# Performance work log

Measured on AMD Instinct MI355X. Metric: run time of the kernel, lower is better.

## Reference

```python
import jax, jax.numpy as jnp
import numpy as np

NV, NR = 30000, 1000
EVV, EVI, EIV = 400000, 120000, 120000
VD, RD, ED = 16, 8, 2
HID, OUT, H1 = 64, 64, 2


def _seg_softmax(logits, seg, n):
    # numerically stable segment softmax over destination nodes
    m = jax.ops.segment_max(logits, seg, num_segments=n)
    m = jnp.where(jnp.isfinite(m), m, 0.0)
    ex = jnp.exp(logits - m[seg])
    den = jax.ops.segment_sum(ex, seg, num_segments=n)
    return ex / (den[seg] + 1e-16)


def _gatv2(x_src, x_dst, src, dst, ea, Wl, Wr, We, att, b, heads, n_dst, concat):
    # PyG GATv2Conv: e = att . leaky_relu(Wl x_j + Wr x_i + We e_ij); out = sum_j softmax(e) * Wl x_j
    C = att.shape[-1]
    hl = (x_src @ Wl).reshape(-1, heads, C)
    hr = (x_dst @ Wr).reshape(-1, heads, C)
    he = (ea @ We).reshape(-1, heads, C)
    xj = hl[src]                                   # [E, H, C]
    g = jax.nn.leaky_relu(xj + hr[dst] + he, 0.2)
    logits = jnp.einsum('ehc,hc->eh', g, att)      # [E, H]
    alpha = _seg_softmax(logits, dst, n_dst)
    out = jax.ops.segment_sum(xj * alpha[..., None], dst, num_segments=n_dst)
    out = out.reshape(n_dst, heads * C) if concat else out.mean(axis=1)
    return out + b


def _self_loops(src, dst, ea, n):
    # PyG add_self_loops(fill_value='mean'): self-loop edge_attr = per-dst mean of incoming edge_attr
    deg = jax.ops.segment_sum(jnp.ones((ea.shape[0],), ea.dtype), dst, num_segments=n)
    mean = jax.ops.segment_sum(ea, dst, num_segments=n) / jnp.maximum(deg, 1.0)[:, None]
    ar = jnp.arange(n, dtype=src.dtype)
    return jnp.concatenate([src, ar]), jnp.concatenate([dst, ar]), jnp.concatenate([ea, mean], axis=0)


def _ln(x, g, b):
    m = x.mean(-1, keepdims=True)
    v = ((x - m) ** 2).mean(-1, keepdims=True)
    return (x - m) * jax.lax.rsqrt(v + 1e-5) * g + b


def setup_inputs() -> dict:
    key = jax.random.key(0)
    ks = iter(jax.random.split(key, 80))
    def rn(shape, s=1.0):
        return jax.random.normal(next(ks), shape, jnp.float32) * s
    def ri(n, hi):
        return jax.random.randint(next(ks), (n,), 0, hi, jnp.int32)
    d = {'x_veh': rn((NV, VD)), 'x_rsu': rn((NR, RD)),
         'ea_v2v': rn((EVV, ED)), 'ea_v2i': rn((EVI, ED)), 'ea_i2v': rn((EIV, ED)),
         'src_v2v': ri(EVV, NV), 'dst_v2v': ri(EVV, NV),
         'src_v2i': ri(EVI, NV), 'dst_v2i': ri(EVI, NR),
         'src_i2v': ri(EIV, NR), 'dst_i2v': ri(EIV, NV)}
    H1C = H1 * HID
    for rel, di_s, di_d in (('vv', VD, VD), ('vi', VD, RD), ('iv', RD, VD)):
        d['Wl_' + rel + '1'] = rn((di_s, H1C), 0.1)
        d['Wr_' + rel + '1'] = rn((di_d, H1C), 0.1)
        d['We_' + rel + '1'] = rn((ED, H1C), 0.1)
        d['att_' + rel + '1'] = rn((H1, HID), 0.1)
        d['b_' + rel + '1'] = jnp.zeros((H1C,), jnp.float32)
    for rel in ('vv', 'vi', 'iv'):
        d['Wl_' + rel + '2'] = rn((H1C, OUT), 0.1)
        d['Wr_' + rel + '2'] = rn((H1C, OUT), 0.1)
        d['We_' + rel + '2'] = rn((ED, OUT), 0.1)
        d['att_' + rel + '2'] = rn((1, OUT), 0.1)
        d['b_' + rel + '2'] = jnp.zeros((OUT,), jnp.float32)
    d['ln_vg'] = jnp.ones((OUT,), jnp.float32)
    d['ln_vb'] = jnp.zeros((OUT,), jnp.float32)
    d['ln_rg'] = jnp.ones((OUT,), jnp.float32)
    d['ln_rb'] = jnp.zeros((OUT,), jnp.float32)
    return d


def reference(x_veh, x_rsu, ea_v2v, ea_v2i, ea_i2v,
              src_v2v, dst_v2v, src_v2i, dst_v2i, src_i2v, dst_i2v,
              Wl_vv1, Wr_vv1, We_vv1, att_vv1, b_vv1,
              Wl_vi1, Wr_vi1, We_vi1, att_vi1, b_vi1,
              Wl_iv1, Wr_iv1, We_iv1, att_iv1, b_iv1,
              Wl_vv2, Wr_vv2, We_vv2, att_vv2, b_vv2,
              Wl_vi2, Wr_vi2, We_vi2, att_vi2, b_vi2,
              Wl_iv2, Wr_iv2, We_iv2, att_iv2, b_iv2,
              ln_vg, ln_vb, ln_rg, ln_rb):
    s_vv, d_vv, ea_vv = _self_loops(src_v2v, dst_v2v, ea_v2v, NV)
    # layer 1 (heads=2, concat=True), HeteroConv aggr='sum'
    v1 = (_gatv2(x_veh, x_veh, s_vv, d_vv, ea_vv, Wl_vv1, Wr_vv1, We_vv1, att_vv1, b_vv1, H1, NV, True)
          + _gatv2(x_rsu, x_veh, src_i2v, dst_i2v, ea_i2v, Wl_iv1, Wr_iv1, We_iv1, att_iv1, b_iv1, H1, NV, True))
    r1 = _gatv2(x_veh, x_rsu, src_v2i, dst_v2i, ea_v2i, Wl_vi1, Wr_vi1, We_vi1, att_vi1, b_vi1, H1, NR, True)
    v1 = jax.nn.elu(v1)
    r1 = jax.nn.elu(r1)
    # layer 2 (heads=1, concat=False -> mean over 1 head)
    v2 = (_gatv2(v1, v1, s_vv, d_vv, ea_vv, Wl_vv2, Wr_vv2, We_vv2, att_vv2, b_vv2, 1, NV, False)
          + _gatv2(r1, v1, src_i2v, dst_i2v, ea_i2v, Wl_iv2, Wr_iv2, We_iv2, att_iv2, b_iv2, 1, NV, False))
    r2 = _gatv2(v1, r1, src_v2i, dst_v2i, ea_v2i, Wl_vi2, Wr_vi2, We_vi2, att_vi2, b_vi2, 1, NR, False)
    return jnp.concatenate([_ln(v2, ln_vg, ln_vb), _ln(r2, ln_rg, ln_rb)], axis=0)
```

## Files before the change

### kernel.cpp

```cpp
#include <hip/hip_runtime.h>
#include <hip/hip_fp16.h>

constexpr int NV = 30000, NR = 1000;
constexpr int EVV = 400000, EVI = 120000, EIV = 120000;
constexpr int ETOT = EVV + EIV + EVI;
constexpr int VB = (NV + 3) / 4;
constexpr float LOFF = 4.0f;

struct __align__(8) Edge { int s; __half2 ea; };
typedef __half2 h2;

__device__ __forceinline__ h2 h2shfl_xor(h2 v, int m) {
  int i = *(int*)&v;
  i = __shfl_xor(i, m);
  return *(h2*)&i;
}
__device__ __forceinline__ h2 h2max(h2 a, h2 b) {
  h2 r;
  asm("v_pk_max_f16 %0, %1, %2" : "=v"(r) : "v"(a), "v"(b));
  return r;
}

constexpr size_t OFF_CNT_VV = 0;
constexpr size_t OFF_CUR_VV = OFF_CNT_VV + NV;
constexpr size_t OFF_CNT_IV = OFF_CUR_VV + NV;
constexpr size_t OFF_CUR_IV = OFF_CNT_IV + NV;
constexpr size_t OFF_CNT_VI = OFF_CUR_IV + NV;
constexpr size_t OFF_CUR_VI = OFF_CNT_VI + NR;
constexpr size_t ZERO_END   = OFF_CUR_VI + NR;
constexpr size_t OFF_PTR_VV = ZERO_END;
constexpr size_t OFF_PTR_IV = OFF_PTR_VV + NV + 2;
constexpr size_t OFF_PTR_VI = OFF_PTR_IV + NV + 2;
constexpr size_t OFF_E_VV   = OFF_PTR_VI + NR + 2;
constexpr size_t OFF_E_IV   = OFF_E_VV + (size_t)EVV * 2;
constexpr size_t OFF_E_VI   = OFF_E_IV + (size_t)EIV * 2;
constexpr size_t OFF_H      = (OFF_E_VI + (size_t)EVI * 2 + 3) & ~(size_t)3;
constexpr size_t OFF_HL_VV1 = OFF_H;
constexpr size_t OFF_HR_VV1 = OFF_HL_VV1 + (size_t)NV * 64;
constexpr size_t OFF_HR_IV1 = OFF_HR_VV1 + (size_t)NV * 64;
constexpr size_t OFF_HL_VI1 = OFF_HR_IV1 + (size_t)NV * 64;
constexpr size_t OFF_HL_IV1 = OFF_HL_VI1 + (size_t)NV * 64;
constexpr size_t OFF_HR_VI1 = OFF_HL_IV1 + (size_t)NR * 64;
constexpr size_t L1_END     = OFF_HR_VI1 + (size_t)NR * 64;
constexpr size_t OFF_V1     = L1_END;
constexpr size_t OFF_R1     = OFF_V1 + (size_t)NV * 64;
constexpr size_t WS_END     = OFF_R1 + (size_t)NR * 64;
constexpr size_t OFF_HL_VV2 = OFF_H;
constexpr size_t OFF_HR_VV2 = OFF_HL_VV2 + (size_t)NV * 32;
constexpr size_t OFF_HR_IV2 = OFF_HR_VV2 + (size_t)NV * 32;
constexpr size_t OFF_HL_VI2 = OFF_HR_IV2 + (size_t)NV * 32;
constexpr size_t OFF_HL_IV2 = OFF_HL_VI2 + (size_t)NV * 32;
constexpr size_t OFF_HR_VI2 = OFF_HL_IV2 + (size_t)NR * 32;
constexpr size_t L2_END     = OFF_HR_VI2 + (size_t)NR * 32;
static_assert(L2_END <= OFF_V1, "layer-2 overlay must not clobber v1/r1");

__global__ __launch_bounds__(256) void k_count3(
    const int* __restrict__ dvv, const int* __restrict__ div_, const int* __restrict__ dvi,
    int* __restrict__ cvv, int* __restrict__ civ, int* __restrict__ cvi) {
  int t = blockIdx.x * blockDim.x + threadIdx.x;
  if (t < EVV) atomicAdd(&cvv[dvv[t]], 1);
  else if (t < EVV + EIV) atomicAdd(&civ[div_[t - EVV]], 1);
  else if (t < ETOT) atomicAdd(&cvi[dvi[t - EVV - EIV]], 1);
}

__global__ __launch_bounds__(1024) void k_scan3(
    const int* c0, int* p0, int n0,
    const int* c1, int* p1, int n1,
    const int* c2, int* p2, int n2) {
  const int* cnt = blockIdx.x == 0 ? c0 : blockIdx.x == 1 ? c1 : c2;
  int* ptr = blockIdx.x == 0 ? p0 : blockIdx.x == 1 ? p1 : p2;
  int n = blockIdx.x == 0 ? n0 : blockIdx.x == 1 ? n1 : n2;
  __shared__ int tsum[1024];
  int t = threadIdx.x;
  int per = (n + 1023) >> 10;
  int base = t * per;
  int s = 0;
  for (int i = 0; i < per; i++) { int idx = base + i; if (idx < n) s += cnt[idx]; }
  tsum[t] = s;
  for (int off = 1; off < 1024; off <<= 1) {
    __syncthreads();
    int v = (t >= off) ? tsum[t - off] : 0;
    __syncthreads();
    tsum[t] += v;
  }
  __syncthreads();
  int run = tsum[t] - s;
  for (int i = 0; i < per; i++) {
    int idx = base + i;
    if (idx < n) { ptr[idx] = run; run += cnt[idx]; }
  }
  if (t == 1023) ptr[n] = tsum[1023];
}

__global__ __launch_bounds__(256) void k_fill3(
    const int* __restrict__ svv, const int* __restrict__ dvv, const float* __restrict__ eavv,
    const int* __restrict__ siv, const int* __restrict__ div_, const float* __restrict__ eaiv,
    const int* __restrict__ svi, const int* __restrict__ dvi, const float* __restrict__ eavi,
    const int* __restrict__ pvv, int* __restrict__ uvv, Edge* __restrict__ evv,
    const int* __restrict__ piv, int* __restrict__ uiv, Edge* __restrict__ eiv,
    const int* __restrict__ pvi, int* __restrict__ uvi, Edge* __restrict__ evi) {
  int t = blockIdx.x * blockDim.x + threadIdx.x;
  if (t < EVV) {
    int e = t, d = dvv[e];
    int idx = pvv[d] + atomicAdd(&uvv[d], 1);
    Edge ed; ed.s = svv[e]; ed.ea = __floats2half2_rn(eavv[2 * e], eavv[2 * e + 1]);
    evv[idx] = ed;
  } else if (t < EVV + EIV) {
    int e = t - EVV, d = div_[e];
    int idx = piv[d] + atomicAdd(&uiv[d], 1);
    Edge ed; ed.s = siv[e]; ed.ea = __floats2half2_rn(eaiv[2 * e], eaiv[2 * e + 1]);
    eiv[idx] = ed;
  } else if (t < ETOT) {
    int e = t - EVV - EIV, d = dvi[e];
    int idx = pvi[d] + atomicAdd(&uvi[d], 1);
    Edge ed; ed.s = svi[e]; ed.ea = __floats2half2_rn(eavi[2 * e], eavi[2 * e + 1]);
    evi[idx] = ed;
  }
}

template<int K, int NW>
__global__ __launch_bounds__(256) void k_gemm1(const float* __restrict__ X,
    const float* __restrict__ W0, const float* __restrict__ W1,
    const float* __restrict__ W2, const float* __restrict__ W3,
    __half* __restrict__ Y0, __half* __restrict__ Y1,
    __half* __restrict__ Y2, __half* __restrict__ Y3, int n) {
  constexpr int ROWS = 8;
  __shared__ float xs[ROWS][K];
  int r0 = blockIdx.x * ROWS;
  int tid = threadIdx.x;
  int col = tid & 127, grp = tid >> 7;
  for (int i = tid; i < ROWS * K; i += 256) {
    int gi = r0 * K + i;
    ((float*)xs)[i] = (gi < n * K) ? X[gi] : 0.f;
  }
  __syncthreads();
  int oidx = ((col & 63) << 1) + (col >> 6);
#pragma unroll
  for (int rep = 0; rep < NW / 2; rep++) {
    int wi = grp + rep * 2;
    const float* __restrict__ W = wi == 0 ? W0 : wi == 1 ? W1 : wi == 2 ? W2 : W3;
    __half* __restrict__ Y = wi == 0 ? Y0 : wi == 1 ? Y1 : wi == 2 ? Y2 : Y3;
    float acc[ROWS];
#pragma unroll
    for (int r = 0; r < ROWS; r++) acc[r] = 0.f;
#pragma unroll
    for (int k4 = 0; k4 < K / 4; k4++) {
      float w0 = W[(4 * k4 + 0) * 128 + col];
      float w1 = W[(4 * k4 + 1) * 128 + col];
      float w2 = W[(4 * k4 + 2) * 128 + col];
      float w3 = W[(4 * k4 + 3) * 128 + col];
#pragma unroll
      for (int r = 0; r < ROWS; r++) {
        float4 x4 = *(const float4*)&xs[r][4 * k4];
        acc[r] = fmaf(x4.x, w0, acc[r]);
        acc[r] = fmaf(x4.y, w1, acc[r]);
        acc[r] = fmaf(x4.z, w2, acc[r]);
        acc[r] = fmaf(x4.w, w3, acc[r]);
      }
    }
#pragma unroll
    for (int r = 0; r < ROWS; r++)
      if (r0 + r < n) Y[(size_t)(r0 + r) * 128 + oidx] = __float2half(acc[r]);
  }
}

template<int NW>
__global__ __launch_bounds__(64 * NW) void k_gemm2(const __half* __restrict__ X,
    const float* __restrict__ W0, const float* __restrict__ W1,
    const float* __restrict__ W2, const float* __restrict__ W3,
    __half* __restrict__ Y0, __half* __restrict__ Y1,
    __half* __restrict__ Y2, __half* __restrict__ Y3, int n) {
  constexpr int ROWS = 16, K = 128;
  __shared__ float xs[ROWS][K];
  int r0 = blockIdx.x * ROWS;
  int tid = threadIdx.x;
  const __half2* X2 = (const __half2*)X;
  for (int i = tid; i < ROWS * K / 2; i += 64 * NW) {
    int gi = r0 * (K / 2) + i;
    float2 f = (gi < n * (K / 2)) ? __half22float2(X2[gi]) : make_float2(0.f, 0.f);
    ((float*)xs)[2 * i] = f.x;
    ((float*)xs)[2 * i + 1] = f.y;
  }
  __syncthreads();
  int lane = tid & 63, wv = tid >> 6;
  const float* __restrict__ W = wv == 0 ? W0 : wv == 1 ? W1 : wv == 2 ? W2 : W3;
  __half* __restrict__ Y = wv == 0 ? Y0 : wv == 1 ? Y1 : wv == 2 ? Y2 : Y3;
  float acc[ROWS];
#pragma unroll
  for (int r = 0; r < ROWS; r++) acc[r] = 0.f;
  for (int k4 = 0; k4 < K / 4; k4++) {
    float w0 = W[(4 * k4 + 0) * 64 + lane];
    float w1 = W[(4 * k4 + 1) * 64 + lane];
    float w2 = W[(4 * k4 + 2) * 64 + lane];
    float w3 = W[(4 * k4 + 3) * 64 + lane];
#pragma unroll
    for (int r = 0; r < ROWS; r++) {
      float4 x4 = *(const float4*)&xs[r][4 * k4];
      acc[r] = fmaf(x4.x, w0, acc[r]);
      acc[r] = fmaf(x4.y, w1, acc[r]);
      acc[r] = fmaf(x4.z, w2, acc[r]);
      acc[r] = fmaf(x4.w, w3, acc[r]);
    }
  }
#pragma unroll
  for (int r = 0; r < ROWS; r++)
    if (r0 + r < n) Y[(size_t)(r0 + r) * 64 + lane] = __float2half(acc[r]);
}


template<bool SELF>
__device__ __forceinline__ void gatW2(int d, int lane, int eg, int cg,
    int b, int cnt,
    const Edge* __restrict__ ed,
    const __half* __restrict__ hl, const __half* __restrict__ hr,
    const float* __restrict__ We, const float* __restrict__ att,
    float* acc, float& den0, float& den1) {
  h2 hrc2[4], av2[4], w02[4], w12[4];
  {
    float4 r = *(const float4*)&hr[(size_t)d * 128 + cg * 8];
    const h2* hp = (const h2*)&r;
#pragma unroll
    for (int j = 0; j < 4; j++) hrc2[j] = hp[j];
  }
#pragma unroll
  for (int j = 0; j < 4; j++) {
    int c = cg * 4 + j;
    av2[j] = __floats2half2_rn(att[c], att[64 + c]);
    w02[j] = __floats2half2_rn(We[c], We[64 + c]);
    w12[j] = __floats2half2_rn(We[128 + c], We[192 + c]);
  }
  const h2 c02 = __float2half2_rn(0.2f);
  h2 acc2[4];
#pragma unroll
  for (int j = 0; j < 4; j++) acc2[j] = __float2half2_rn(0.f);
  float sum0 = 0.f, sum1 = 0.f;
  auto proc = [&](float4 r, int eab, bool v) {
    const h2* hp = (const h2*)&r;
    h2 eh = *(h2*)&eab;
    h2 ef0 = __low2half2(eh), ef1 = __high2half2(eh);
    h2 lacc = __float2half2_rn(0.f);
#pragma unroll
    for (int j = 0; j < 4; j++) {
      h2 g = __hfma2(ef0, w02[j], __hadd2(hp[j], hrc2[j]));
      g = __hfma2(ef1, w12[j], g);
      h2 lr = h2max(g, __hmul2(c02, g));
      lacc = __hfma2(lr, av2[j], lacc);
    }
#pragma unroll
    for (int o = 1; o <= 8; o <<= 1) lacc = __hadd2(lacc, h2shfl_xor(lacc, o));
    float2 lf = __half22float2(lacc);
    float ex0 = v ? __expf(lf.x - LOFF) : 0.f;
    float ex1 = v ? __expf(lf.y - LOFF) : 0.f;
    h2 exh = __floats2half2_rn(ex0, ex1);
#pragma unroll
    for (int j = 0; j < 4; j++) acc2[j] = __hfma2(exh, hp[j], acc2[j]);
    den0 += ex0; den1 += ex1;
  };
  for (int wf = 0; wf < cnt; wf += 64) {
    int idx = wf + lane;
    int es = 0, eab = 0;
    if (idx < cnt) { Edge e = ed[b + idx]; es = e.s; eab = *(const int*)&e.ea; }
    if (SELF) {
      float2 f = __half22float2(*(h2*)&eab);
      sum0 += f.x; sum1 += f.y;
    }
    int wlen = min(64, cnt - wf);
    int kk = 0;
    for (; kk + 16 <= wlen; kk += 16) {
      int k0 = kk + eg, k1 = kk + 4 + eg, k2 = kk + 8 + eg, k3 = kk + 12 + eg;
      int s0 = __shfl(es, k0), ea0 = __shfl(eab, k0);
      int s1 = __shfl(es, k1), ea1 = __shfl(eab, k1);
      int s2 = __shfl(es, k2), ea2 = __shfl(eab, k2);
      int s3 = __shfl(es, k3), ea3 = __shfl(eab, k3);
      float4 r0 = *(const float4*)&hl[(size_t)s0 * 128 + cg * 8];
      float4 r1 = *(const float4*)&hl[(size_t)s1 * 128 + cg * 8];
      float4 r2 = *(const float4*)&hl[(size_t)s2 * 128 + cg * 8];
      float4 r3 = *(const float4*)&hl[(size_t)s3 * 128 + cg * 8];
      proc(r0, ea0, true);
      proc(r1, ea1, true);
      proc(r2, ea2, true);
      proc(r3, ea3, true);
    }
    for (; kk < wlen; kk += 4) {
      int k0 = kk + eg;
      int s0 = __shfl(es, k0), ea0 = __shfl(eab, k0);
      float4 r0 = *(const float4*)&hl[(size_t)s0 * 128 + cg * 8];
      proc(r0, ea0, k0 < wlen);
    }
  }
  if (SELF) {
#pragma unroll
    for (int o = 1; o <= 32; o <<= 1) { sum0 += __shfl_xor(sum0, o); sum1 += __shfl_xor(sum1, o); }
    float dg = fmaxf((float)cnt, 1.f);
    __half2 mh = __floats2half2_rn(sum0 / dg, sum1 / dg);
    int meab = *(const int*)&mh;
    float4 rS = *(const float4*)&hl[(size_t)d * 128 + cg * 8];
    proc(rS, meab, eg == 0);
  }
#pragma unroll
  for (int o = 16; o <= 32; o <<= 1) {
#pragma unroll
    for (int j = 0; j < 4; j++) acc2[j] = __hadd2(acc2[j], h2shfl_xor(acc2[j], o));
    den0 += __shfl_xor(den0, o);
    den1 += __shfl_xor(den1, o);
  }
#pragma unroll
  for (int j = 0; j < 4; j++) {
    float2 f = __half22float2(acc2[j]);
    acc[2 * j] = f.x; acc[2 * j + 1] = f.y;
  }
}

template<bool SELF>
__device__ __forceinline__ void gatW1(int d, int lane, int eg8, int cg8,
    int b, int cnt,
    const Edge* __restrict__ ed,
    const __half* __restrict__ hl, const __half* __restrict__ hr,
    const float* __restrict__ We, const float* __restrict__ att,
    float* acc, float& den) {
  h2 hrc2[4], av2[4], w02[4], w12[4];
  {
    float4 r = *(const float4*)&hr[(size_t)d * 64 + cg8 * 8];
    const h2* hp = (const h2*)&r;
#pragma unroll
    for (int j = 0; j < 4; j++) hrc2[j] = hp[j];
  }
#pragma unroll
  for (int j = 0; j < 4; j++) {
    int c = cg8 * 8 + 2 * j;
    av2[j] = __floats2half2_rn(att[c], att[c + 1]);
    w02[j] = __floats2half2_rn(We[c], We[c + 1]);
    w12[j] = __floats2half2_rn(We[64 + c], We[64 + c + 1]);
  }
  const h2 c02 = __float2half2_rn(0.2f);
  h2 acc2[4];
#pragma unroll
  for (int j = 0; j < 4; j++) acc2[j] = __float2half2_rn(0.f);
  float sum0 = 0.f, sum1 = 0.f;
  auto proc = [&](float4 r, int eab, bool v) {
    const h2* hp = (const h2*)&r;
    h2 eh = *(h2*)&eab;
    h2 ef0 = __low2half2(eh), ef1 = __high2half2(eh);
    h2 lacc = __float2half2_rn(0.f);
#pragma unroll
    for (int j = 0; j < 4; j++) {
      h2 g = __hfma2(ef0, w02[j], __hadd2(hp[j], hrc2[j]));
      g = __hfma2(ef1, w12[j], g);
      h2 lr = h2max(g, __hmul2(c02, g));
      lacc = __hfma2(lr, av2[j], lacc);
    }
#pragma unroll
    for (int o = 1; o <= 4; o <<= 1) lacc = __hadd2(lacc, h2shfl_xor(lacc, o));
    float2 lf = __half22float2(lacc);
    float ex = v ? __expf(lf.x + lf.y - LOFF) : 0.f;
    h2 exh = __float2half2_rn(ex);
#pragma unroll
    for (int j = 0; j < 4; j++) acc2[j] = __hfma2(exh, hp[j], acc2[j]);
    den += ex;
  };
  for (int wf = 0; wf < cnt; wf += 64) {
    int idx = wf + lane;
    int es = 0, eab = 0;
    if (idx < cnt) { Edge e = ed[b + idx]; es = e.s; eab = *(const int*)&e.ea; }
    if (SELF) {
      float2 f = __half22float2(*(h2*)&eab);
      sum0 += f.x; sum1 += f.y;
    }
    int wlen = min(64, cnt - wf);
    int kk = 0;
    for (; kk + 32 <= wlen; kk += 32) {
      int k0 = kk + eg8, k1 = kk + 8 + eg8, k2 = kk + 16 + eg8, k3 = kk + 24 + eg8;
      int s0 = __shfl(es, k0), ea0 = __shfl(eab, k0);
      int s1 = __shfl(es, k1), ea1 = __shfl(eab, k1);
      int s2 = __shfl(es, k2), ea2 = __shfl(eab, k2);
      int s3 = __shfl(es, k3), ea3 = __shfl(eab, k3);
      float4 r0 = *(const float4*)&hl[(size_t)s0 * 64 + cg8 * 8];
      float4 r1 = *(const float4*)&hl[(size_t)s1 * 64 + cg8 * 8];
      float4 r2 = *(const float4*)&hl[(size_t)s2 * 64 + cg8 * 8];
      float4 r3 = *(const float4*)&hl[(size_t)s3 * 64 + cg8 * 8];
      proc(r0, ea0, true);
      proc(r1, ea1, true);
      proc(r2, ea2, true);
      proc(r3, ea3, true);
    }
    for (; kk < wlen; kk += 8) {
      int k0 = kk + eg8;
      int s0 = __shfl(es, k0), ea0 = __shfl(eab, k0);
      float4 r0 = *(const float4*)&hl[(size_t)s0 * 64 + cg8 * 8];
      proc(r0, ea0, k0 < wlen);
    }
  }
  if (SELF) {
#pragma unroll
    for (int o = 1; o <= 32; o <<= 1) { sum0 += __shfl_xor(sum0, o); sum1 += __shfl_xor(sum1, o); }
    float dg = fmaxf((float)cnt, 1.f);
    __half2 mh = __floats2half2_rn(sum0 / dg, sum1 / dg);
    int meab = *(const int*)&mh;
    float4 rS = *(const float4*)&hl[(size_t)d * 64 + cg8 * 8];
    proc(rS, meab, eg8 == 0);
  }
#pragma unroll
  for (int o = 8; o <= 32; o <<= 1) {
#pragma unroll
    for (int j = 0; j < 4; j++) acc2[j] = __hadd2(acc2[j], h2shfl_xor(acc2[j], o));
    den += __shfl_xor(den, o);
  }
#pragma unroll
  for (int j = 0; j < 4; j++) {
    float2 f = __half22float2(acc2[j]);
    acc[2 * j] = f.x; acc[2 * j + 1] = f.y;
  }
}

__global__ __launch_bounds__(256) void k_gat_l1(
    const int* ptr_vv, const Edge* e_vv,
    const __half* hl_vv, const __half* hr_vv, const float* We_vv, const float* att_vv,
    const int* ptr_iv, const Edge* e_iv,
    const __half* hl_iv, const __half* hr_iv, const float* We_iv, const float* att_iv,
    const int* ptr_vi, const Edge* e_vi,
    const __half* hl_vi, const __half* hr_vi, const float* We_vi, const float* att_vi,
    const float* b_vv, const float* b_iv, const float* b_vi,
    __half* __restrict__ v1, __half* __restrict__ r1) {
  __shared__ float sm[4][16][10];
  int lane = threadIdx.x & 63, wv = threadIdx.x >> 6;
  int eg = lane >> 4, cg = lane & 15;
  if (blockIdx.x >= NR) {
    int w = (blockIdx.x - NR) * 4 + wv;
    if (w >= NV) return;
    float acc[8];
    float d0 = 0.f, d1 = 0.f, oc[8];
    int b = ptr_vv[w], cnt = ptr_vv[w + 1] - b;
    gatW2<true>(w, lane, eg, cg, b, cnt, e_vv, hl_vv, hr_vv, We_vv, att_vv, acc, d0, d1);
#pragma unroll
    for (int j = 0; j < 8; j++) oc[j] = acc[j] / (((j & 1) ? d1 : d0) + 1e-16f);
    d0 = d1 = 0.f;
    b = ptr_iv[w]; cnt = ptr_iv[w + 1] - b;
    gatW2<false>(w, lane, eg, cg, b, cnt, e_iv, hl_iv, hr_iv, We_iv, att_iv, acc, d0, d1);
#pragma unroll
    for (int j = 0; j < 8; j++) oc[j] += acc[j] / (((j & 1) ? d1 : d0) + 1e-16f);
    if (eg == 0) {
      float x[8];
#pragma unroll
      for (int j = 0; j < 8; j++) {
        int c = cg * 4 + (j >> 1);
        int idx = (j & 1) * 64 + c;
        float v = oc[j] + b_vv[idx] + b_iv[idx];
        x[j] = v > 0.f ? v : __expf(v) - 1.f;
      }
      __half2 h0a = __floats2half2_rn(x[0], x[2]), h0b = __floats2half2_rn(x[4], x[6]);
      __half2 h1a = __floats2half2_rn(x[1], x[3]), h1b = __floats2half2_rn(x[5], x[7]);
      float2 p0, p1;
      ((__half2*)&p0)[0] = h0a; ((__half2*)&p0)[1] = h0b;
      ((__half2*)&p1)[0] = h1a; ((__half2*)&p1)[1] = h1b;
      *(float2*)&v1[(size_t)w * 128 + cg * 4]      = p0;
      *(float2*)&v1[(size_t)w * 128 + 64 + cg * 4] = p1;
    }
  } else {
    int dd = blockIdx.x;
    int bfull = ptr_vi[dd], cntf = ptr_vi[dd + 1] - bfull;
    int q = (cntf + 3) >> 2;
    int off = min(wv * q, cntf);
    int cnt = min(q, cntf - off);
    float acc[8];
    float d0 = 0.f, d1 = 0.f;
    gatW2<false>(dd, lane, eg, cg, bfull + off, cnt, e_vi, hl_vi, hr_vi, We_vi, att_vi, acc, d0, d1);
    if (eg == 0) {
#pragma unroll
      for (int j = 0; j < 8; j++) sm[wv][cg][j] = acc[j];
      sm[wv][cg][8] = d0; sm[wv][cg][9] = d1;
    }
    __syncthreads();
    if (wv == 0) {
#pragma unroll
      for (int j = 0; j < 8; j++)
        acc[j] = sm[0][cg][j] + sm[1][cg][j] + sm[2][cg][j] + sm[3][cg][j];
      d0 = sm[0][cg][8] + sm[1][cg][8] + sm[2][cg][8] + sm[3][cg][8];
      d1 = sm[0][cg][9] + sm[1][cg][9] + sm[2][cg][9] + sm[3][cg][9];
      if (eg == 0) {
        float x[8];
#pragma unroll
        for (int j = 0; j < 8; j++) {
          int c = cg * 4 + (j >> 1);
          int idx = (j & 1) * 64 + c;
          float v = acc[j] / (((j & 1) ? d1 : d0) + 1e-16f) + b_vi[idx];
          x[j] = v > 0.f ? v : __expf(v) - 1.f;
        }
        __half2 h0a = __floats2half2_rn(x[0], x[2]), h0b = __floats2half2_rn(x[4], x[6]);
        __half2 h1a = __floats2half2_rn(x[1], x[3]), h1b = __floats2half2_rn(x[5], x[7]);
        float2 p0, p1;
        ((__half2*)&p0)[0] = h0a; ((__half2*)&p0)[1] = h0b;
        ((__half2*)&p1)[0] = h1a; ((__half2*)&p1)[1] = h1b;
        *(float2*)&r1[(size_t)dd * 128 + cg * 4]      = p0;
        *(float2*)&r1[(size_t)dd * 128 + 64 + cg * 4] = p1;
      }
    }
  }
}

__global__ __launch_bounds__(256) void k_gat_l2(
    const int* ptr_vv, const Edge* e_vv,
    const __half* hl_vv, const __half* hr_vv, const float* We_vv, const float* att_vv,
    const int* ptr_iv, const Edge* e_iv,
    const __half* hl_iv, const __half* hr_iv, const float* We_iv, const float* att_iv,
    const int* ptr_vi, const Edge* e_vi,
    const __half* hl_vi, const __half* hr_vi, const float* We_vi, const float* att_vi,
    const float* b_vv, const float* b_iv, const float* b_vi,
    const float* ln_vg, const float* ln_vb, const float* ln_rg, const float* ln_rb,
    float* __restrict__ out) {
  __shared__ float sm[4][8][9];
  int lane = threadIdx.x & 63, wv = threadIdx.x >> 6;
  int eg8 = lane >> 3, cg8 = lane & 7;
  if (blockIdx.x >= NR) {
    int w = (blockIdx.x - NR) * 4 + wv;
    if (w >= NV) return;
    float acc[8];
    float dn = 0.f, oc[8];
    int b = ptr_vv[w], cnt = ptr_vv[w + 1] - b;
    gatW1<true>(w, lane, eg8, cg8, b, cnt, e_vv, hl_vv, hr_vv, We_vv, att_vv, acc, dn);
#pragma unroll
    for (int j = 0; j < 8; j++) oc[j] = acc[j] / (dn + 1e-16f);
    dn = 0.f;
    b = ptr_iv[w]; cnt = ptr_iv[w + 1] - b;
    gatW1<false>(w, lane, eg8, cg8, b, cnt, e_iv, hl_iv, hr_iv, We_iv, att_iv, acc, dn);
    float x[8], s = 0.f;
#pragma unroll
    for (int j = 0; j < 8; j++) {
      int c = cg8 * 8 + j;
      x[j] = oc[j] + acc[j] / (dn + 1e-16f) + b_vv[c] + b_iv[c];
      s += x[j];
    }
#pragma unroll
    for (int o = 1; o <= 4; o <<= 1) s += __shfl_xor(s, o);
    float mu = s * (1.f / 64.f);
    float v = 0.f;
#pragma unroll
    for (int j = 0; j < 8; j++) { float dx = x[j] - mu; v = fmaf(dx, dx, v); }
#pragma unroll
    for (int o = 1; o <= 4; o <<= 1) v += __shfl_xor(v, o);
    float rstd = rsqrtf(v * (1.f / 64.f) + 1e-5f);
    if (eg8 == 0) {
      float4 o0, o1;
      float* ov = (float*)&o0;
#pragma unroll
      for (int j = 0; j < 4; j++) {
        int c = cg8 * 8 + j;
        ov[j] = (x[j] - mu) * rstd * ln_vg[c] + ln_vb[c];
      }
      ov = (float*)&o1;
#pragma unroll
      for (int j = 0; j < 4; j++) {
        int c = cg8 * 8 + 4 + j;
        ov[j] = (x[4 + j] - mu) * rstd * ln_vg[c] + ln_vb[c];
      }
      *(float4*)&out[(size_t)w * 64 + cg8 * 8]     = o0;
      *(float4*)&out[(size_t)w * 64 + cg8 * 8 + 4] = o1;
    }
  } else {
    int dd = blockIdx.x;
    int bfull = ptr_vi[dd], cntf = ptr_vi[dd + 1] - bfull;
    int q = (cntf + 3) >> 2;
    int off = min(wv * q, cntf);
    int cnt = min(q, cntf - off);
    float acc[8];
    float dn = 0.f;
    gatW1<false>(dd, lane, eg8, cg8, bfull + off, cnt, e_vi, hl_vi, hr_vi, We_vi, att_vi, acc, dn);
    if (eg8 == 0) {
#pragma unroll
      for (int j = 0; j < 8; j++) sm[wv][cg8][j] = acc[j];
      sm[wv][cg8][8] = dn;
    }
    __syncthreads();
    if (wv == 0) {
#pragma unroll
      for (int j = 0; j < 8; j++)
        acc[j] = sm[0][cg8][j] + sm[1][cg8][j] + sm[2][cg8][j] + sm[3][cg8][j];
      dn = sm[0][cg8][8] + sm[1][cg8][8] + sm[2][cg8][8] + sm[3][cg8][8];
      float x[8], s = 0.f;
#pragma unroll
      for (int j = 0; j < 8; j++) {
        int c = cg8 * 8 + j;
        x[j] = acc[j] / (dn + 1e-16f) + b_vi[c];
        s += x[j];
      }
#pragma unroll
      for (int o = 1; o <= 4; o <<= 1) s += __shfl_xor(s, o);
      float mu = s * (1.f / 64.f);
      float v = 0.f;
#pragma unroll
      for (int j = 0; j < 8; j++) { float dx = x[j] - mu; v = fmaf(dx, dx, v); }
#pragma unroll
      for (int o = 1; o <= 4; o <<= 1) v += __shfl_xor(v, o);
      float rstd = rsqrtf(v * (1.f / 64.f) + 1e-5f);
      if (eg8 == 0) {
#pragma unroll
        for (int j = 0; j < 8; j++) {
          int c = cg8 * 8 + j;
          out[(size_t)(NV + dd) * 64 + c] = (x[j] - mu) * rstd * ln_rg[c] + ln_rb[c];
        }
      }
    }
  }
}

extern "C" void kernel_launch(void* const* d_in, const int* in_sizes, int n_in,
                              void* d_out, int out_size, void* d_ws, size_t ws_size,
                              hipStream_t stream) {
  const float* x_veh  = (const float*)d_in[0];
  const float* x_rsu  = (const float*)d_in[1];
  const float* ea_vv  = (const float*)d_in[2];
  const float* ea_vi  = (const float*)d_in[3];
  const float* ea_iv  = (const float*)d_in[4];
  const int*   src_vv = (const int*)d_in[5];
  const int*   dst_vv = (const int*)d_in[6];
  const int*   src_vi = (const int*)d_in[7];
  const int*   dst_vi = (const int*)d_in[8];
  const int*   src_iv = (const int*)d_in[9];
  const int*   dst_iv = (const int*)d_in[10];
  const float* Wl_vv1 = (const float*)d_in[11];
  const float* Wr_vv1 = (const float*)d_in[12];
  const float* We_vv1 = (const float*)d_in[13];
  const float* att_vv1= (const float*)d_in[14];
  const float* b_vv1  = (const float*)d_in[15];
  const float* Wl_vi1 = (const float*)d_in[16];
  const float* Wr_vi1 = (const float*)d_in[17];
  const float* We_vi1 = (const float*)d_in[18];
  const float* att_vi1= (const float*)d_in[19];
  const float* b_vi1  = (const float*)d_in[20];
  const float* Wl_iv1 = (const float*)d_in[21];
  const float* Wr_iv1 = (const float*)d_in[22];
  const float* We_iv1 = (const float*)d_in[23];
  const float* att_iv1= (const float*)d_in[24];
  const float* b_iv1  = (const float*)d_in[25];
  const float* Wl_vv2 = (const float*)d_in[26];
  const float* Wr_vv2 = (const float*)d_in[27];
  const float* We_vv2 = (const float*)d_in[28];
  const float* att_vv2= (const float*)d_in[29];
  const float* b_vv2  = (const float*)d_in[30];
  const float* Wl_vi2 = (const float*)d_in[31];
  const float* Wr_vi2 = (const float*)d_in[32];
  const float* We_vi2 = (const float*)d_in[33];
  const float* att_vi2= (const float*)d_in[34];
  const float* b_vi2  = (const float*)d_in[35];
  const float* Wl_iv2 = (const float*)d_in[36];
  const float* Wr_iv2 = (const float*)d_in[37];
  const float* We_iv2 = (const float*)d_in[38];
  const float* att_iv2= (const float*)d_in[39];
  const float* b_iv2  = (const float*)d_in[40];
  const float* ln_vg  = (const float*)d_in[41];
  const float* ln_vb  = (const float*)d_in[42];
  const float* ln_rg  = (const float*)d_in[43];
  const float* ln_rb  = (const float*)d_in[44];

  float* ws  = (float*)d_ws;
  float* out = (float*)d_out;

  int* cnt_vv = (int*)(ws + OFF_CNT_VV); int* cur_vv = (int*)(ws + OFF_CUR_VV);
  int* cnt_iv = (int*)(ws + OFF_CNT_IV); int* cur_iv = (int*)(ws + OFF_CUR_IV);
  int* cnt_vi = (int*)(ws + OFF_CNT_VI); int* cur_vi = (int*)(ws + OFF_CUR_VI);
  int* ptr_vv = (int*)(ws + OFF_PTR_VV);
  int* ptr_iv = (int*)(ws + OFF_PTR_IV);
  int* ptr_vi = (int*)(ws + OFF_PTR_VI);
  Edge* e_vv = (Edge*)(ws + OFF_E_VV);
  Edge* e_iv = (Edge*)(ws + OFF_E_IV);
  Edge* e_vi = (Edge*)(ws + OFF_E_VI);

  __half* hl_vv1 = (__half*)(ws + OFF_HL_VV1);
  __half* hr_vv1 = (__half*)(ws + OFF_HR_VV1);
  __half* hr_iv1 = (__half*)(ws + OFF_HR_IV1);
  __half* hl_vi1 = (__half*)(ws + OFF_HL_VI1);
  __half* hl_iv1 = (__half*)(ws + OFF_HL_IV1);
  __half* hr_vi1 = (__half*)(ws + OFF_HR_VI1);
  __half* v1 = (__half*)(ws + OFF_V1);
  __half* r1 = (__half*)(ws + OFF_R1);
  __half* hl_vv2 = (__half*)(ws + OFF_HL_VV2);
  __half* hr_vv2 = (__half*)(ws + OFF_HR_VV2);
  __half* hr_iv2 = (__half*)(ws + OFF_HR_IV2);
  __half* hl_vi2 = (__half*)(ws + OFF_HL_VI2);
  __half* hl_iv2 = (__half*)(ws + OFF_HL_IV2);
  __half* hr_vi2 = (__half*)(ws + OFF_HR_VI2);

  (void)hipMemsetAsync(ws, 0, ZERO_END * sizeof(float), stream);

  k_count3<<<(ETOT + 255) / 256, 256, 0, stream>>>(dst_vv, dst_iv, dst_vi,
      cnt_vv, cnt_iv, cnt_vi);
  k_scan3<<<3, 1024, 0, stream>>>(cnt_vv, ptr_vv, NV, cnt_iv, ptr_iv, NV, cnt_vi, ptr_vi, NR);
  k_fill3<<<(ETOT + 255) / 256, 256, 0, stream>>>(
      src_vv, dst_vv, ea_vv, src_iv, dst_iv, ea_iv, src_vi, dst_vi, ea_vi,
      ptr_vv, cur_vv, e_vv, ptr_iv, cur_iv, e_iv, ptr_vi, cur_vi, e_vi);

  k_gemm1<16, 4><<<(NV + 7) / 8, 256, 0, stream>>>(x_veh,
      Wl_vv1, Wr_vv1, Wr_iv1, Wl_vi1, hl_vv1, hr_vv1, hr_iv1, hl_vi1, NV);
  k_gemm1<8, 2><<<(NR + 7) / 8, 256, 0, stream>>>(x_rsu,
      Wl_iv1, Wr_vi1, nullptr, nullptr, hl_iv1, hr_vi1, nullptr, nullptr, NR);

  k_gat_l1<<<NR + VB, 256, 0, stream>>>(
      ptr_vv, e_vv, hl_vv1, hr_vv1, We_vv1, att_vv1,
      ptr_iv, e_iv, hl_iv1, hr_iv1, We_iv1, att_iv1,
      ptr_vi, e_vi, hl_vi1, hr_vi1, We_vi1, att_vi1,
      b_vv1, b_iv1, b_vi1, v1, r1);

  k_gemm2<4><<<(NV + 15) / 16, 256, 0, stream>>>(v1,
      Wl_vv2, Wr_vv2, Wr_iv2, Wl_vi2, hl_vv2, hr_vv2, hr_iv2, hl_vi2, NV);
  k_gemm2<2><<<(NR + 15) / 16, 128, 0, stream>>>(r1,
      Wl_iv2, Wr_vi2, nullptr, nullptr, hl_iv2, hr_vi2, nullptr, nullptr, NR);

  k_gat_l2<<<NR + VB, 256, 0, stream>>>(
      ptr_vv, e_vv, hl_vv2, hr_vv2, We_vv2, att_vv2,
      ptr_iv, e_iv, hl_iv2, hr_iv2, We_iv2, att_iv2,
      ptr_vi, e_vi, hl_vi2, hr_vi2, We_vi2, att_vi2,
      b_vv2, b_iv2, b_vi2, ln_vg, ln_vb, ln_rg, ln_rb, out);
  (void)in_sizes; (void)n_in; (void)out_size; (void)ws_size;
}
```

Measured before the change: 360.2 us.

## Record per-edge rank in count pass and hoist first edge-window loads

The CSR build now takes each edge's rank from the counting atomic and stores it in a temporary record with src, dst and the half-precision edge attribute. The fill pass then scatters without a second atomic and without rereading the raw inputs. The GAT kernels also issue the first 64-edge window loads and the hr row loads for both relations before any compute starts, so those loads can overlap. The cost is an extra 16-byte-per-edge temporary buffer written and read back, plus higher register pressure from the values held early.

```diff
diff --git a/kernel.cpp b/kernel.cpp
--- a/kernel.cpp
+++ b/kernel.cpp
@@ -8,6 +8,7 @@
 constexpr float LOFF = 4.0f;
 
 struct __align__(8) Edge { int s; __half2 ea; };
+struct __align__(16) TRec { int s; int d; __half2 ea; int r; };
 typedef __half2 h2;
 
 __device__ __forceinline__ h2 h2shfl_xor(h2 v, int m) {
@@ -21,20 +22,18 @@
   return r;
 }
 
-constexpr size_t OFF_CNT_VV = 0;
-constexpr size_t OFF_CUR_VV = OFF_CNT_VV + NV;
-constexpr size_t OFF_CNT_IV = OFF_CUR_VV + NV;
-constexpr size_t OFF_CUR_IV = OFF_CNT_IV + NV;
-constexpr size_t OFF_CNT_VI = OFF_CUR_IV + NV;
-constexpr size_t OFF_CUR_VI = OFF_CNT_VI + NR;
+constexpr size_t OFF_CUR_VV = 0;
+constexpr size_t OFF_CUR_IV = OFF_CUR_VV + NV;
+constexpr size_t OFF_CUR_VI = OFF_CUR_IV + NV;
 constexpr size_t ZERO_END   = OFF_CUR_VI + NR;
 constexpr size_t OFF_PTR_VV = ZERO_END;
 constexpr size_t OFF_PTR_IV = OFF_PTR_VV + NV + 2;
 constexpr size_t OFF_PTR_VI = OFF_PTR_IV + NV + 2;
-constexpr size_t OFF_E_VV   = OFF_PTR_VI + NR + 2;
+constexpr size_t OFF_E_VV   = (OFF_PTR_VI + NR + 2 + 3) & ~(size_t)3;
 constexpr size_t OFF_E_IV   = OFF_E_VV + (size_t)EVV * 2;
 constexpr size_t OFF_E_VI   = OFF_E_IV + (size_t)EIV * 2;
-constexpr size_t OFF_H      = (OFF_E_VI + (size_t)EVI * 2 + 3) & ~(size_t)3;
+constexpr size_t OFF_TMP    = (OFF_E_VI + (size_t)EVI * 2 + 3) & ~(size_t)3;
+constexpr size_t OFF_H      = (OFF_TMP + (size_t)ETOT * 4 + 3) & ~(size_t)3;
 constexpr size_t OFF_HL_VV1 = OFF_H;
 constexpr size_t OFF_HR_VV1 = OFF_HL_VV1 + (size_t)NV * 64;
 constexpr size_t OFF_HR_IV1 = OFF_HR_VV1 + (size_t)NV * 64;
@@ -54,13 +53,32 @@
 constexpr size_t L2_END     = OFF_HR_VI2 + (size_t)NR * 32;
 static_assert(L2_END <= OFF_V1, "layer-2 overlay must not clobber v1/r1");
 
-__global__ __launch_bounds__(256) void k_count3(
-    const int* __restrict__ dvv, const int* __restrict__ div_, const int* __restrict__ dvi,
-    int* __restrict__ cvv, int* __restrict__ civ, int* __restrict__ cvi) {
+__global__ __launch_bounds__(256) void k_build1(
+    const int* __restrict__ svv, const int* __restrict__ dvv, const float* __restrict__ eavv,
+    const int* __restrict__ siv, const int* __restrict__ div_, const float* __restrict__ eaiv,
+    const int* __restrict__ svi, const int* __restrict__ dvi, const float* __restrict__ eavi,
+    int* __restrict__ cvv, int* __restrict__ civ, int* __restrict__ cvi,
+    TRec* __restrict__ tmp) {
   int t = blockIdx.x * blockDim.x + threadIdx.x;
-  if (t < EVV) atomicAdd(&cvv[dvv[t]], 1);
-  else if (t < EVV + EIV) atomicAdd(&civ[div_[t - EVV]], 1);
-  else if (t < ETOT) atomicAdd(&cvi[dvi[t - EVV - EIV]], 1);
+  if (t < EVV) {
+    int d = dvv[t];
+    TRec rec; rec.s = svv[t]; rec.d = d;
+    rec.ea = __floats2half2_rn(eavv[2 * t], eavv[2 * t + 1]);
+    rec.r = atomicAdd(&cvv[d], 1);
+    tmp[t] = rec;
+  } else if (t < EVV + EIV) {
+    int e = t - EVV, d = div_[e];
+    TRec rec; rec.s = siv[e]; rec.d = d;
+    rec.ea = __floats2half2_rn(eaiv[2 * e], eaiv[2 * e + 1]);
+    rec.r = atomicAdd(&civ[d], 1);
+    tmp[t] = rec;
+  } else if (t < ETOT) {
+    int e = t - EVV - EIV, d = dvi[e];
+    TRec rec; rec.s = svi[e]; rec.d = d;
+    rec.ea = __floats2half2_rn(eavi[2 * e], eavi[2 * e + 1]);
+    rec.r = atomicAdd(&cvi[d], 1);
+    tmp[t] = rec;
+  }
 }
 
 __global__ __launch_bounds__(1024) void k_scan3(
@@ -92,30 +110,17 @@
   if (t == 1023) ptr[n] = tsum[1023];
 }
 
-__global__ __launch_bounds__(256) void k_fill3(
-    const int* __restrict__ svv, const int* __restrict__ dvv, const float* __restrict__ eavv,
-    const int* __restrict__ siv, const int* __restrict__ div_, const float* __restrict__ eaiv,
-    const int* __restrict__ svi, const int* __restrict__ dvi, const float* __restrict__ eavi,
-    const int* __restrict__ pvv, int* __restrict__ uvv, Edge* __restrict__ evv,
-    const int* __restrict__ piv, int* __restrict__ uiv, Edge* __restrict__ eiv,
-    const int* __restrict__ pvi, int* __restrict__ uvi, Edge* __restrict__ evi) {
+__global__ __launch_bounds__(256) void k_build2(
+    const TRec* __restrict__ tmp,
+    const int* __restrict__ pvv, const int* __restrict__ piv, const int* __restrict__ pvi,
+    Edge* __restrict__ evv, Edge* __restrict__ eiv, Edge* __restrict__ evi) {
   int t = blockIdx.x * blockDim.x + threadIdx.x;
-  if (t < EVV) {
-    int e = t, d = dvv[e];
-    int idx = pvv[d] + atomicAdd(&uvv[d], 1);
-    Edge ed; ed.s = svv[e]; ed.ea = __floats2half2_rn(eavv[2 * e], eavv[2 * e + 1]);
-    evv[idx] = ed;
-  } else if (t < EVV + EIV) {
-    int e = t - EVV, d = div_[e];
-    int idx = piv[d] + atomicAdd(&uiv[d], 1);
-    Edge ed; ed.s = siv[e]; ed.ea = __floats2half2_rn(eaiv[2 * e], eaiv[2 * e + 1]);
-    eiv[idx] = ed;
-  } else if (t < ETOT) {
-    int e = t - EVV - EIV, d = dvi[e];
-    int idx = pvi[d] + atomicAdd(&uvi[d], 1);
-    Edge ed; ed.s = svi[e]; ed.ea = __floats2half2_rn(eavi[2 * e], eavi[2 * e + 1]);
-    evi[idx] = ed;
-  }
+  if (t >= ETOT) return;
+  TRec rec = tmp[t];
+  Edge ed; ed.s = rec.s; ed.ea = rec.ea;
+  if (t < EVV)            evv[pvv[rec.d] + rec.r] = ed;
+  else if (t < EVV + EIV) eiv[piv[rec.d] + rec.r] = ed;
+  else                    evi[pvi[rec.d] + rec.r] = ed;
 }
 
 template<int K, int NW>
@@ -210,18 +215,15 @@
 
 template<bool SELF>
 __device__ __forceinline__ void gatW2(int d, int lane, int eg, int cg,
-    int b, int cnt,
+    int b, int cnt, int es0, int eab0,
     const Edge* __restrict__ ed,
-    const __half* __restrict__ hl, const __half* __restrict__ hr,
+    const __half* __restrict__ hl, float4 hrr,
     const float* __restrict__ We, const float* __restrict__ att,
     float* acc, float& den0, float& den1) {
   h2 hrc2[4], av2[4], w02[4], w12[4];
-  {
-    float4 r = *(const float4*)&hr[(size_t)d * 128 + cg * 8];
-    const h2* hp = (const h2*)&r;
-#pragma unroll
-    for (int j = 0; j < 4; j++) hrc2[j] = hp[j];
-  }
+  const h2* hrp = (const h2*)&hrr;
+#pragma unroll
+  for (int j = 0; j < 4; j++) hrc2[j] = hrp[j];
 #pragma unroll
   for (int j = 0; j < 4; j++) {
     int c = cg * 4 + j;
@@ -256,15 +258,7 @@
     for (int j = 0; j < 4; j++) acc2[j] = __hfma2(exh, hp[j], acc2[j]);
     den0 += ex0; den1 += ex1;
   };
-  for (int wf = 0; wf < cnt; wf += 64) {
-    int idx = wf + lane;
-    int es = 0, eab = 0;
-    if (idx < cnt) { Edge e = ed[b + idx]; es = e.s; eab = *(const int*)&e.ea; }
-    if (SELF) {
-      float2 f = __half22float2(*(h2*)&eab);
-      sum0 += f.x; sum1 += f.y;
-    }
-    int wlen = min(64, cnt - wf);
+  auto doWin = [&](int es, int eab, int wlen) {
     int kk = 0;
     for (; kk + 16 <= wlen; kk += 16) {
       int k0 = kk + eg, k1 = kk + 4 + eg, k2 = kk + 8 + eg, k3 = kk + 12 + eg;
@@ -287,6 +281,21 @@
       float4 r0 = *(const float4*)&hl[(size_t)s0 * 128 + cg * 8];
       proc(r0, ea0, k0 < wlen);
     }
+  };
+  if (SELF) {
+    float2 f = __half22float2(*(h2*)&eab0);
+    sum0 += f.x; sum1 += f.y;
+  }
+  doWin(es0, eab0, min(64, cnt));
+  for (int wf = 64; wf < cnt; wf += 64) {
+    int idx = wf + lane;
+    int es = 0, eab = 0;
+    if (idx < cnt) { Edge e = ed[b + idx]; es = e.s; eab = *(const int*)&e.ea; }
+    if (SELF) {
+      float2 f = __half22float2(*(h2*)&eab);
+      sum0 += f.x; sum1 += f.y;
+    }
+    doWin(es, eab, min(64, cnt - wf));
   }
   if (SELF) {
 #pragma unroll
@@ -313,18 +322,15 @@
 
 template<bool SELF>
 __device__ __forceinline__ void gatW1(int d, int lane, int eg8, int cg8,
-    int b, int cnt,
+    int b, int cnt, int es0, int eab0,
     const Edge* __restrict__ ed,
-    const __half* __restrict__ hl, const __half* __restrict__ hr,
+    const __half* __restrict__ hl, float4 hrr,
     const float* __restrict__ We, const float* __restrict__ att,
     float* acc, float& den) {
   h2 hrc2[4], av2[4], w02[4], w12[4];
-  {
-    float4 r = *(const float4*)&hr[(size_t)d * 64 + cg8 * 8];
-    const h2* hp = (const h2*)&r;
-#pragma unroll
-    for (int j = 0; j < 4; j++) hrc2[j] = hp[j];
-  }
+  const h2* hrp = (const h2*)&hrr;
+#pragma unroll
+  for (int j = 0; j < 4; j++) hrc2[j] = hrp[j];
 #pragma unroll
   for (int j = 0; j < 4; j++) {
     int c = cg8 * 8 + 2 * j;
@@ -358,15 +364,7 @@
     for (int j = 0; j < 4; j++) acc2[j] = __hfma2(exh, hp[j], acc2[j]);
     den += ex;
   };
-  for (int wf = 0; wf < cnt; wf += 64) {
-    int idx = wf + lane;
-    int es = 0, eab = 0;
-    if (idx < cnt) { Edge e = ed[b + idx]; es = e.s; eab = *(const int*)&e.ea; }
-    if (SELF) {
-      float2 f = __half22float2(*(h2*)&eab);
-      sum0 += f.x; sum1 += f.y;
-    }
-    int wlen = min(64, cnt - wf);
+  auto doWin = [&](int es, int eab, int wlen) {
     int kk = 0;
     for (; kk + 32 <= wlen; kk += 32) {
       int k0 = kk + eg8, k1 = kk + 8 + eg8, k2 = kk + 16 + eg8, k3 = kk + 24 + eg8;
@@ -389,6 +387,21 @@
       float4 r0 = *(const float4*)&hl[(size_t)s0 * 64 + cg8 * 8];
       proc(r0, ea0, k0 < wlen);
     }
+  };
+  if (SELF) {
+    float2 f = __half22float2(*(h2*)&eab0);
+    sum0 += f.x; sum1 += f.y;
+  }
+  doWin(es0, eab0, min(64, cnt));
+  for (int wf = 64; wf < cnt; wf += 64) {
+    int idx = wf + lane;
+    int es = 0, eab = 0;
+    if (idx < cnt) { Edge e = ed[b + idx]; es = e.s; eab = *(const int*)&e.ea; }
+    if (SELF) {
+      float2 f = __half22float2(*(h2*)&eab);
+      sum0 += f.x; sum1 += f.y;
+    }
+    doWin(es, eab, min(64, cnt - wf));
   }
   if (SELF) {
 #pragma unroll
@@ -427,15 +440,20 @@
   if (blockIdx.x >= NR) {
     int w = (blockIdx.x - NR) * 4 + wv;
     if (w >= NV) return;
+    int b1 = ptr_vv[w], c1 = ptr_vv[w + 1] - b1;
+    int b2 = ptr_iv[w], c2 = ptr_iv[w + 1] - b2;
+    int es1 = 0, ea1 = 0, es2 = 0, ea2 = 0;
+    if (lane < c1) { Edge e = e_vv[b1 + lane]; es1 = e.s; ea1 = *(const int*)&e.ea; }
+    if (lane < c2) { Edge e = e_iv[b2 + lane]; es2 = e.s; ea2 = *(const int*)&e.ea; }
+    float4 hrv = *(const float4*)&hr_vv[(size_t)w * 128 + cg * 8];
+    float4 hri = *(const float4*)&hr_iv[(size_t)w * 128 + cg * 8];
     float acc[8];
     float d0 = 0.f, d1 = 0.f, oc[8];
-    int b = ptr_vv[w], cnt = ptr_vv[w + 1] - b;
-    gatW2<true>(w, lane, eg, cg, b, cnt, e_vv, hl_vv, hr_vv, We_vv, att_vv, acc, d0, d1);
+    gatW2<true>(w, lane, eg, cg, b1, c1, es1, ea1, e_vv, hl_vv, hrv, We_vv, att_vv, acc, d0, d1);
 #pragma unroll
     for (int j = 0; j < 8; j++) oc[j] = acc[j] / (((j & 1) ? d1 : d0) + 1e-16f);
     d0 = d1 = 0.f;
-    b = ptr_iv[w]; cnt = ptr_iv[w + 1] - b;
-    gatW2<false>(w, lane, eg, cg, b, cnt, e_iv, hl_iv, hr_iv, We_iv, att_iv, acc, d0, d1);
+    gatW2<false>(w, lane, eg, cg, b2, c2, es2, ea2, e_iv, hl_iv, hri, We_iv, att_iv, acc, d0, d1);
 #pragma unroll
     for (int j = 0; j < 8; j++) oc[j] += acc[j] / (((j & 1) ? d1 : d0) + 1e-16f);
     if (eg == 0) {
@@ -461,9 +479,13 @@
     int q = (cntf + 3) >> 2;
     int off = min(wv * q, cntf);
     int cnt = min(q, cntf - off);
+    int b = bfull + off;
+    int es0 = 0, ea0 = 0;
+    if (lane < cnt) { Edge e = e_vi[b + lane]; es0 = e.s; ea0 = *(const int*)&e.ea; }
+    float4 hrr = *(const float4*)&hr_vi[(size_t)dd * 128 + cg * 8];
     float acc[8];
     float d0 = 0.f, d1 = 0.f;
-    gatW2<false>(dd, lane, eg, cg, bfull + off, cnt, e_vi, hl_vi, hr_vi, We_vi, att_vi, acc, d0, d1);
+    gatW2<false>(dd, lane, eg, cg, b, cnt, es0, ea0, e_vi, hl_vi, hrr, We_vi, att_vi, acc, d0, d1);
     if (eg == 0) {
 #pragma unroll
       for (int j = 0; j < 8; j++) sm[wv][cg][j] = acc[j];
@@ -513,15 +535,20 @@
   if (blockIdx.x >= NR) {
     int w = (blockIdx.x - NR) * 4 + wv;
     if (w >= NV) return;
+    int b1 = ptr_vv[w], c1 = ptr_vv[w + 1] - b1;
+    int b2 = ptr_iv[w], c2 = ptr_iv[w + 1] - b2;
+    int es1 = 0, ea1 = 0, es2 = 0, ea2 = 0;
+    if (lane < c1) { Edge e = e_vv[b1 + lane]; es1 = e.s; ea1 = *(const int*)&e.ea; }
+    if (lane < c2) { Edge e = e_iv[b2 + lane]; es2 = e.s; ea2 = *(const int*)&e.ea; }
+    float4 hrv = *(const float4*)&hr_vv[(size_t)w * 64 + cg8 * 8];
+    float4 hri = *(const float4*)&hr_iv[(size_t)w * 64 + cg8 * 8];
     float acc[8];
     float dn = 0.f, oc[8];
-    int b = ptr_vv[w], cnt = ptr_vv[w + 1] - b;
-    gatW1<true>(w, lane, eg8, cg8, b, cnt, e_vv, hl_vv, hr_vv, We_vv, att_vv, acc, dn);
+    gatW1<true>(w, lane, eg8, cg8, b1, c1, es1, ea1, e_vv, hl_vv, hrv, We_vv, att_vv, acc, dn);
 #pragma unroll
     for (int j = 0; j < 8; j++) oc[j] = acc[j] / (dn + 1e-16f);
     dn = 0.f;
-    b = ptr_iv[w]; cnt = ptr_iv[w + 1] - b;
-    gatW1<false>(w, lane, eg8, cg8, b, cnt, e_iv, hl_iv, hr_iv, We_iv, att_iv, acc, dn);
+    gatW1<false>(w, lane, eg8, cg8, b2, c2, es2, ea2, e_iv, hl_iv, hri, We_iv, att_iv, acc, dn);
     float x[8], s = 0.f;
 #pragma unroll
     for (int j = 0; j < 8; j++) {
@@ -561,9 +588,13 @@
     int q = (cntf + 3) >> 2;
     int off = min(wv * q, cntf);
     int cnt = min(q, cntf - off);
+    int b = bfull + off;
+    int es0 = 0, ea0 = 0;
+    if (lane < cnt) { Edge e = e_vi[b + lane]; es0 = e.s; ea0 = *(const int*)&e.ea; }
+    float4 hrr = *(const float4*)&hr_vi[(size_t)dd * 64 + cg8 * 8];
     float acc[8];
     float dn = 0.f;
-    gatW1<false>(dd, lane, eg8, cg8, bfull + off, cnt, e_vi, hl_vi, hr_vi, We_vi, att_vi, acc, dn);
+    gatW1<false>(dd, lane, eg8, cg8, b, cnt, es0, ea0, e_vi, hl_vi, hrr, We_vi, att_vi, acc, dn);
     if (eg8 == 0) {
 #pragma unroll
       for (int j = 0; j < 8; j++) sm[wv][cg8][j] = acc[j];
@@ -654,15 +685,16 @@
   float* ws  = (float*)d_ws;
   float* out = (float*)d_out;
 
-  int* cnt_vv = (int*)(ws + OFF_CNT_VV); int* cur_vv = (int*)(ws + OFF_CUR_VV);
-  int* cnt_iv = (int*)(ws + OFF_CNT_IV); int* cur_iv = (int*)(ws + OFF_CUR_IV);
-  int* cnt_vi = (int*)(ws + OFF_CNT_VI); int* cur_vi = (int*)(ws + OFF_CUR_VI);
+  int* cur_vv = (int*)(ws + OFF_CUR_VV);
+  int* cur_iv = (int*)(ws + OFF_CUR_IV);
+  int* cur_vi = (int*)(ws + OFF_CUR_VI);
   int* ptr_vv = (int*)(ws + OFF_PTR_VV);
   int* ptr_iv = (int*)(ws + OFF_PTR_IV);
   int* ptr_vi = (int*)(ws + OFF_PTR_VI);
   Edge* e_vv = (Edge*)(ws + OFF_E_VV);
   Edge* e_iv = (Edge*)(ws + OFF_E_IV);
   Edge* e_vi = (Edge*)(ws + OFF_E_VI);
+  TRec* tmp  = (TRec*)(ws + OFF_TMP);
 
   __half* hl_vv1 = (__half*)(ws + OFF_HL_VV1);
   __half* hr_vv1 = (__half*)(ws + OFF_HR_VV1);
@@ -681,12 +713,12 @@
 
   (void)hipMemsetAsync(ws, 0, ZERO_END * sizeof(float), stream);
 
-  k_count3<<<(ETOT + 255) / 256, 256, 0, stream>>>(dst_vv, dst_iv, dst_vi,
-      cnt_vv, cnt_iv, cnt_vi);
-  k_scan3<<<3, 1024, 0, stream>>>(cnt_vv, ptr_vv, NV, cnt_iv, ptr_iv, NV, cnt_vi, ptr_vi, NR);
-  k_fill3<<<(ETOT + 255) / 256, 256, 0, stream>>>(
+  k_build1<<<(ETOT + 255) / 256, 256, 0, stream>>>(
       src_vv, dst_vv, ea_vv, src_iv, dst_iv, ea_iv, src_vi, dst_vi, ea_vi,
-      ptr_vv, cur_vv, e_vv, ptr_iv, cur_iv, e_iv, ptr_vi, cur_vi, e_vi);
+      cur_vv, cur_iv, cur_vi, tmp);
+  k_scan3<<<3, 1024, 0, stream>>>(cur_vv, ptr_vv, NV, cur_iv, ptr_iv, NV, cur_vi, ptr_vi, NR);
+  k_build2<<<(ETOT + 255) / 256, 256, 0, stream>>>(tmp, ptr_vv, ptr_iv, ptr_vi,
+      e_vv, e_iv, e_vi);
 
   k_gemm1<16, 4><<<(NV + 7) / 8, 256, 0, stream>>>(x_veh,
       Wl_vv1, Wr_vv1, Wr_iv1, Wl_vi1, hl_vv1, hr_vv1, hr_iv1, hl_vi1, NV);
```

New measurement: 317.6 us. 1.13x faster.
